# Performance work log

Hardware: AMD Instinct MI355X
Metric: run time of the kernel (lower is better)

The kernel has to match this reference:

```python
import jax, jax.numpy as jnp
import numpy as np

B = 8
M = 500_000
XSIZE = 128


def setup_inputs() -> dict:
    key = jax.random.key(0)
    k1, k2 = jax.random.split(key)
    indices = jax.random.randint(k1, (B, M, 3), 0, XSIZE, dtype=jnp.int32)
    values = jax.random.normal(k2, (B, M), dtype=jnp.float32)
    return {"indices": indices, "values": values, "xsize": XSIZE}


def reference(indices, values, xsize):
    # Batched scatter-add density accumulation (tensor_scatter_nd_add per sample)
    def scatter_one(idx, val):
        grid = jnp.zeros((xsize, xsize, xsize), dtype=val.dtype)
        return grid.at[idx[:, 0], idx[:, 1], idx[:, 2]].add(val)

    grid = jax.vmap(scatter_one)(indices, values)  # (B, X, X, X)

    # Adjacent voxel differences along each spatial axis
    d1 = grid[:, 1:, :, :] - grid[:, :-1, :, :]
    d2 = grid[:, :, 1:, :] - grid[:, :, :-1, :]
    d3 = grid[:, :, :, 1:] - grid[:, :, :, :-1]

    ax = (1, 2, 3)
    # Total variation loss: normalized by total voxel count xsize^3
    num_pixels = jnp.float32(xsize * xsize * xsize)
    tv = (jnp.sum(jnp.abs(d1), axis=ax)
          + jnp.sum(jnp.abs(d2), axis=ax)
          + jnp.sum(jnp.abs(d3), axis=ax)) / num_pixels

    # MSE smoothness loss: normalizer matches TF code (2*X*X - X - X)
    num_pairs = jnp.float32(2 * xsize * xsize - 2 * xsize)
    mse = (jnp.sum(jnp.square(d1), axis=ax)
           + jnp.sum(jnp.square(d2), axis=ax)
           + jnp.sum(jnp.square(d3), axis=ax)) / num_pairs

    return jnp.stack([tv, mse])  # (2, B)
```

## Files before the change

kernel.cpp:

```cpp
#include <hip/hip_runtime.h>
#include <stdint.h>

#define BATCH 8
#define MPTS 500000
#define NPTS (BATCH * MPTS)
#define NBQ 1024
#define TP 8192
#define NTILE ((NPTS + TP - 1) / TP)
#define NIFACE 304
#define NBND (BATCH * NIFACE)

template <int NT>
__device__ __forceinline__ void block_reduce2(float& tv, float& mse) {
    for (int off = 32; off > 0; off >>= 1) {
        tv  += __shfl_down(tv, off, 64);
        mse += __shfl_down(mse, off, 64);
    }
    __shared__ float stv[NT / 64], sms[NT / 64];
    int w = threadIdx.x >> 6, lane = threadIdx.x & 63;
    if (lane == 0) { stv[w] = tv; sms[w] = mse; }
    __syncthreads();
    if (threadIdx.x == 0) {
        float a = 0.f, m = 0.f;
        #pragma unroll
        for (int e = 0; e < NT / 64; ++e) { a += stv[e]; m += sms[e]; }
        tv = a; mse = m;
    }
}

__device__ __forceinline__ uint32_t pack_aux(int b, int i, int j, int k) {
    uint32_t q = ((uint32_t)b << 7) | ((uint32_t)(i >> 5) << 5) |
                 ((uint32_t)(j >> 5) << 3) | (uint32_t)(k >> 4);
    uint32_t l = ((uint32_t)(i & 31) << 9) | ((uint32_t)(j & 31) << 4) | (uint32_t)(k & 15);
    return (q << 14) | l;
}

__device__ __forceinline__ int gaddr(int s, int kl) {
    return s * 16 + (kl & 3) + ((((kl >> 2) ^ (s >> 1)) & 3) << 2);
}
__device__ __forceinline__ int goff(int s, int c) {
    return ((c ^ (s >> 1)) & 3) << 2;
}

__global__ void __launch_bounds__(1024) hist_k(const int* __restrict__ idx,
                                               uint32_t* __restrict__ hist,
                                               uint32_t* __restrict__ aux) {
    __shared__ uint32_t h[NBQ];
    h[threadIdx.x] = 0;
    __syncthreads();
    int tile = blockIdx.x;
    int p0 = tile * TP;
    int ng = min(TP, NPTS - p0) >> 2;
    for (int g = threadIdx.x; g < ng; g += 1024) {
        int p = p0 + g * 4;
        const int4* ip = (const int4*)(idx + (size_t)p * 3);
        int4 A = ip[0], B = ip[1], C = ip[2];
        int b = p / MPTS;
        uint32_t a0 = pack_aux(b, A.x, A.y, A.z);
        uint32_t a1 = pack_aux(b, A.w, B.x, B.y);
        uint32_t a2 = pack_aux(b, B.z, B.w, C.x);
        uint32_t a3 = pack_aux(b, C.y, C.z, C.w);
        *(uint4*)(aux + p) = make_uint4(a0, a1, a2, a3);
        atomicAdd(&h[a0 >> 14], 1u);
        atomicAdd(&h[a1 >> 14], 1u);
        atomicAdd(&h[a2 >> 14], 1u);
        atomicAdd(&h[a3 >> 14], 1u);
    }
    __syncthreads();
    hist[(size_t)tile * NBQ + threadIdx.x] = h[threadIdx.x];
}

__global__ void __launch_bounds__(64) scan_tiles_k(uint32_t* __restrict__ hist,
                                                   uint32_t* __restrict__ totals) {
    int q = blockIdx.x * 64 + threadIdx.x;
    uint32_t run = 0;
    for (int t0 = 0; t0 < NTILE; t0 += 16) {
        uint32_t vv[16];
        #pragma unroll
        for (int e = 0; e < 16; ++e) {
            int t = t0 + e;
            vv[e] = (t < NTILE) ? hist[(size_t)t * NBQ + q] : 0u;
        }
        #pragma unroll
        for (int e = 0; e < 16; ++e) {
            int t = t0 + e;
            if (t < NTILE) hist[(size_t)t * NBQ + q] = run;
            run += vv[e];
        }
    }
    totals[q] = run;
}

__global__ void __launch_bounds__(256) scan_base_k(const uint32_t* __restrict__ totals,
                                                   uint32_t* __restrict__ base) {
    __shared__ uint32_t ssum[256];
    uint32_t loc[4];
    int q0 = threadIdx.x * 4;
    uint32_t s = 0;
    #pragma unroll
    for (int e = 0; e < 4; ++e) { loc[e] = totals[q0 + e]; s += loc[e]; }
    ssum[threadIdx.x] = s;
    __syncthreads();
    for (int off = 1; off < 256; off <<= 1) {
        uint32_t v = 0;
        if (threadIdx.x >= off) v = ssum[threadIdx.x - off];
        __syncthreads();
        if (threadIdx.x >= off) ssum[threadIdx.x] += v;
        __syncthreads();
    }
    uint32_t run = threadIdx.x ? ssum[threadIdx.x - 1] : 0;
    #pragma unroll
    for (int e = 0; e < 4; ++e) { base[q0 + e] = run; run += loc[e]; }
}

__global__ void __launch_bounds__(1024, 8) reorder_k(const uint32_t* __restrict__ aux,
                                                     const float* __restrict__ val,
                                                     const uint32_t* __restrict__ hist,
                                                     const uint32_t* __restrict__ base,
                                                     uint32_t* __restrict__ rec) {
    __shared__ uint32_t h[NBQ];
    __shared__ uint32_t gb[NBQ];
    __shared__ uint32_t wtot[16];
    __shared__ uint16_t sq[TP];
    __shared__ uint32_t srt[TP];
    int tile = blockIdx.x;
    int p0 = tile * TP;
    int cnt = min(TP, NPTS - p0);
    h[threadIdx.x] = 0;
    __syncthreads();
    uint32_t a[8]; float v[8];
    #pragma unroll
    for (int e = 0; e < 8; ++e) {
        int r = threadIdx.x + e * 1024;
        if (r < cnt) {
            a[e] = aux[p0 + r];
            v[e] = val[p0 + r];
            atomicAdd(&h[a[e] >> 14], 1u);
        } else a[e] = 0xFFFFFFFFu;
    }
    __syncthreads();
    int q = threadIdx.x, lane = q & 63, wave = q >> 6;
    uint32_t cq = h[q];
    uint32_t inc = cq;
    #pragma unroll
    for (int off = 1; off < 64; off <<= 1) {
        uint32_t n = __shfl_up(inc, off, 64);
        if (lane >= off) inc += n;
    }
    if (lane == 63) wtot[wave] = inc;
    __syncthreads();
    if (q < 16) {
        uint32_t w = wtot[q];
        #pragma unroll
        for (int off = 1; off < 16; off <<= 1) {
            uint32_t n = __shfl_up(w, off, 16);
            if (q >= off) w += n;
        }
        wtot[q] = w;
    }
    __syncthreads();
    uint32_t lstart = (wave ? wtot[wave - 1] : 0u) + inc - cq;
    gb[q] = base[q] + hist[(size_t)tile * NBQ + q] - lstart;
    h[q] = lstart;
    __syncthreads();
    #pragma unroll
    for (int e = 0; e < 8; ++e) {
        if (a[e] != 0xFFFFFFFFu) {
            uint32_t qq = a[e] >> 14;
            uint32_t u = (__float_as_uint(v[e]) + 0x2000u) & 0xFFFFC000u;
            uint32_t pos = atomicAdd(&h[qq], 1u);
            srt[pos] = u | (a[e] & 16383u);
            sq[pos]  = (uint16_t)qq;
        }
    }
    __syncthreads();
    for (int t = threadIdx.x; t < cnt; t += 1024)
        rec[gb[sq[t]] + t] = srt[t];
}

__global__ void __launch_bounds__(1024, 8) accum_k(const uint32_t* __restrict__ rec,
                                                   const uint32_t* __restrict__ base,
                                                   const uint32_t* __restrict__ totals,
                                                   float* __restrict__ faces,
                                                   float2* __restrict__ pa) {
    __shared__ float g[16384];
    int qb = blockIdx.x;
    {
        float4 z = make_float4(0.f, 0.f, 0.f, 0.f);
        #pragma unroll
        for (int c = 0; c < 4; ++c)
            *(float4*)&g[(threadIdx.x + c * 1024) * 4] = z;
    }
    __syncthreads();
    uint32_t s0 = base[qb], cnt = totals[qb];
    for (uint32_t r = threadIdx.x; r < cnt; r += 1024) {
        uint32_t e = rec[s0 + r];
        int l = e & 16383;
        atomicAdd(&g[gaddr(l >> 4, l & 15)], __uint_as_float(e & 0xFFFFC000u));
    }
    __syncthreads();
    float tv = 0.f, mse = 0.f;
    {
        int s = threadIdx.x;
        int jl = s & 31, il = s >> 5;
        bool jin = jl < 31, iin = il < 31;
        float own[16];
        #pragma unroll
        for (int c = 0; c < 4; ++c)
            *(float4*)&own[c * 4] = *(const float4*)&g[s * 16 + goff(s, c)];
        #pragma unroll
        for (int k = 0; k < 15; ++k) {
            float d = own[k + 1] - own[k]; tv += fabsf(d); mse += d * d;
        }
        #pragma unroll
        for (int h = 0; h < 2; ++h) {
            if (jin) {
                float jn[8];
                *(float4*)&jn[0] = *(const float4*)&g[(s + 1) * 16 + goff(s + 1, 2 * h)];
                *(float4*)&jn[4] = *(const float4*)&g[(s + 1) * 16 + goff(s + 1, 2 * h + 1)];
                #pragma unroll
                for (int k = 0; k < 8; ++k) {
                    float d = jn[k] - own[8 * h + k]; tv += fabsf(d); mse += d * d;
                }
            }
            if (iin) {
                float inb[8];
                *(float4*)&inb[0] = *(const float4*)&g[(s + 32) * 16 + goff(s + 32, 2 * h)];
                *(float4*)&inb[4] = *(const float4*)&g[(s + 32) * 16 + goff(s + 32, 2 * h + 1)];
                #pragma unroll
                for (int k = 0; k < 8; ++k) {
                    float d = inb[k] - own[8 * h + k]; tv += fabsf(d); mse += d * d;
                }
            }
        }
    }
    {
        float* f = faces + (size_t)qb * 4096;
        int t = threadIdx.x;
        if (t < 512) {
            int hi = t >> 4, lo = t & 15;
            f[t]        = g[gaddr(hi, lo)];
            f[512 + t]  = g[gaddr(992 + hi, lo)];
            f[1024 + t] = g[gaddr(hi * 32, lo)];
            f[1536 + t] = g[gaddr(hi * 32 + 31, lo)];
        }
        f[2048 + t] = g[gaddr(t, 0)];
        f[3072 + t] = g[gaddr(t, 15)];
    }
    block_reduce2<1024>(tv, mse);
    if (threadIdx.x == 0) pa[qb] = make_float2(tv, mse);
}

__global__ void __launch_bounds__(256) boundary_k(const float* __restrict__ faces,
                                                  float2* __restrict__ pb) {
    int x = blockIdx.x;
    int b = x / NIFACE;
    int r = x - b * NIFACE;
    int qA, qB, fA, fB, elems;
    if (r < 96) {
        int s = r >> 5, u = (r >> 3) & 3, w = r & 7;
        qA = (b << 7) | (s << 5) | (u << 3) | w; qB = qA + 32;
        fA = 512; fB = 0; elems = 512;
    } else if (r < 192) {
        int r2 = r - 96;
        int s = r2 >> 5, u = (r2 >> 3) & 3, w = r2 & 7;
        qA = (b << 7) | (u << 5) | (s << 3) | w; qB = qA + 8;
        fA = 1536; fB = 1024; elems = 512;
    } else {
        int r2 = r - 192;
        int s = r2 >> 4, u = (r2 >> 2) & 3, v = r2 & 3;
        qA = (b << 7) | (u << 5) | (v << 3) | s; qB = qA + 1;
        fA = 3072; fB = 2048; elems = 1024;
    }
    const float* pA = faces + (size_t)qA * 4096 + fA;
    const float* pB = faces + (size_t)qB * 4096 + fB;
    float tv = 0.f, mse = 0.f;
    for (int e = threadIdx.x; e < elems; e += 256) {
        float d = pB[e] - pA[e];
        tv += fabsf(d); mse += d * d;
    }
    block_reduce2<256>(tv, mse);
    if (threadIdx.x == 0) pb[x] = make_float2(tv, mse);
}

__global__ void __launch_bounds__(256) final_k(const float2* __restrict__ pa,
                                               const float2* __restrict__ pb,
                                               float* __restrict__ out) {
    int b = blockIdx.x;
    float tv = 0.f, mse = 0.f;
    const float2* a = pa + (size_t)b * (NBQ / BATCH);
    for (int i = threadIdx.x; i < NBQ / BATCH; i += 256) { float2 v = a[i]; tv += v.x; mse += v.y; }
    const float2* p = pb + (size_t)b * NIFACE;
    for (int i = threadIdx.x; i < NIFACE; i += 256) { float2 v = p[i]; tv += v.x; mse += v.y; }
    block_reduce2<256>(tv, mse);
    if (threadIdx.x == 0) {
        out[b]     = tv  * (1.f / 2097152.f);
        out[8 + b] = mse * (1.f / 32512.f);
    }
}

extern "C" void kernel_launch(void* const* d_in, const int* in_sizes, int n_in,
                              void* d_out, int out_size, void* d_ws, size_t ws_size,
                              hipStream_t stream) {
    const int*   indices = (const int*)d_in[0];
    const float* values  = (const float*)d_in[1];
    float*       out     = (float*)d_out;

    uint32_t* hist   = (uint32_t*)d_ws;
    uint32_t* totals = hist + (size_t)NTILE * NBQ;
    uint32_t* base   = totals + NBQ;
    float2*   pa     = (float2*)(base + NBQ);
    float2*   pb     = pa + NBQ;
    uint32_t* rec    = (uint32_t*)(pb + NBND);
    float*    faces  = (float*)(rec + NPTS);
    uint32_t* aux    = (uint32_t*)faces;

    hist_k      <<<NTILE, 1024, 0, stream>>>(indices, hist, aux);
    scan_tiles_k<<<16,    64,   0, stream>>>(hist, totals);
    scan_base_k <<<1,     256,  0, stream>>>(totals, base);
    reorder_k   <<<NTILE, 1024, 0, stream>>>(aux, values, hist, base, rec);
    accum_k     <<<NBQ,   1024, 0, stream>>>(rec, base, totals, faces, pa);
    boundary_k  <<<NBND,  256,  0, stream>>>(faces, pb);
    final_k     <<<BATCH, 256,  0, stream>>>(pa, pb, out);
}
```

Baseline: 158.3 us.

## Fuse histogram and reorder into tile-local sort, drop global scans

Histogram, two scan kernels and reorder become one sort_k. It sorts each tile locally by bucket in shared memory, writes the tile contiguously with vector stores, and records per-tile bucket offsets. accum_k now gathers each bucket's segments across all tiles: up to 512 tiles, each split between two threads, read sequentially. This removes the aux round trip, the global scans and the scattered writes, and cuts the launch count. In exchange, reads in accum_k become many short per-thread serial loops with uneven lengths.

```diff
diff --git a/kernel.cpp b/kernel.cpp
--- a/kernel.cpp
+++ b/kernel.cpp
@@ -7,6 +7,7 @@
 #define NBQ 1024
 #define TP 8192
 #define NTILE ((NPTS + TP - 1) / TP)
+#define HROW (NBQ + 1)
 #define NIFACE 304
 #define NBND (BATCH * NIFACE)
 
@@ -42,86 +43,12 @@
     return ((c ^ (s >> 1)) & 3) << 2;
 }
 
-__global__ void __launch_bounds__(1024) hist_k(const int* __restrict__ idx,
-                                               uint32_t* __restrict__ hist,
-                                               uint32_t* __restrict__ aux) {
+__global__ void __launch_bounds__(1024, 8) sort_k(const int* __restrict__ idx,
+                                                  const float* __restrict__ val,
+                                                  uint32_t* __restrict__ hoff,
+                                                  uint32_t* __restrict__ rec) {
     __shared__ uint32_t h[NBQ];
-    h[threadIdx.x] = 0;
-    __syncthreads();
-    int tile = blockIdx.x;
-    int p0 = tile * TP;
-    int ng = min(TP, NPTS - p0) >> 2;
-    for (int g = threadIdx.x; g < ng; g += 1024) {
-        int p = p0 + g * 4;
-        const int4* ip = (const int4*)(idx + (size_t)p * 3);
-        int4 A = ip[0], B = ip[1], C = ip[2];
-        int b = p / MPTS;
-        uint32_t a0 = pack_aux(b, A.x, A.y, A.z);
-        uint32_t a1 = pack_aux(b, A.w, B.x, B.y);
-        uint32_t a2 = pack_aux(b, B.z, B.w, C.x);
-        uint32_t a3 = pack_aux(b, C.y, C.z, C.w);
-        *(uint4*)(aux + p) = make_uint4(a0, a1, a2, a3);
-        atomicAdd(&h[a0 >> 14], 1u);
-        atomicAdd(&h[a1 >> 14], 1u);
-        atomicAdd(&h[a2 >> 14], 1u);
-        atomicAdd(&h[a3 >> 14], 1u);
-    }
-    __syncthreads();
-    hist[(size_t)tile * NBQ + threadIdx.x] = h[threadIdx.x];
-}
-
-__global__ void __launch_bounds__(64) scan_tiles_k(uint32_t* __restrict__ hist,
-                                                   uint32_t* __restrict__ totals) {
-    int q = blockIdx.x * 64 + threadIdx.x;
-    uint32_t run = 0;
-    for (int t0 = 0; t0 < NTILE; t0 += 16) {
-        uint32_t vv[16];
-        #pragma unroll
-        for (int e = 0; e < 16; ++e) {
-            int t = t0 + e;
-            vv[e] = (t < NTILE) ? hist[(size_t)t * NBQ + q] : 0u;
-        }
-        #pragma unroll
-        for (int e = 0; e < 16; ++e) {
-            int t = t0 + e;
-            if (t < NTILE) hist[(size_t)t * NBQ + q] = run;
-            run += vv[e];
-        }
-    }
-    totals[q] = run;
-}
-
-__global__ void __launch_bounds__(256) scan_base_k(const uint32_t* __restrict__ totals,
-                                                   uint32_t* __restrict__ base) {
-    __shared__ uint32_t ssum[256];
-    uint32_t loc[4];
-    int q0 = threadIdx.x * 4;
-    uint32_t s = 0;
-    #pragma unroll
-    for (int e = 0; e < 4; ++e) { loc[e] = totals[q0 + e]; s += loc[e]; }
-    ssum[threadIdx.x] = s;
-    __syncthreads();
-    for (int off = 1; off < 256; off <<= 1) {
-        uint32_t v = 0;
-        if (threadIdx.x >= off) v = ssum[threadIdx.x - off];
-        __syncthreads();
-        if (threadIdx.x >= off) ssum[threadIdx.x] += v;
-        __syncthreads();
-    }
-    uint32_t run = threadIdx.x ? ssum[threadIdx.x - 1] : 0;
-    #pragma unroll
-    for (int e = 0; e < 4; ++e) { base[q0 + e] = run; run += loc[e]; }
-}
-
-__global__ void __launch_bounds__(1024, 8) reorder_k(const uint32_t* __restrict__ aux,
-                                                     const float* __restrict__ val,
-                                                     const uint32_t* __restrict__ hist,
-                                                     const uint32_t* __restrict__ base,
-                                                     uint32_t* __restrict__ rec) {
-    __shared__ uint32_t h[NBQ];
-    __shared__ uint32_t gb[NBQ];
     __shared__ uint32_t wtot[16];
-    __shared__ uint16_t sq[TP];
     __shared__ uint32_t srt[TP];
     int tile = blockIdx.x;
     int p0 = tile * TP;
@@ -129,14 +56,25 @@
     h[threadIdx.x] = 0;
     __syncthreads();
     uint32_t a[8]; float v[8];
+    int ng = cnt >> 2;
     #pragma unroll
-    for (int e = 0; e < 8; ++e) {
-        int r = threadIdx.x + e * 1024;
-        if (r < cnt) {
-            a[e] = aux[p0 + r];
-            v[e] = val[p0 + r];
-            atomicAdd(&h[a[e] >> 14], 1u);
-        } else a[e] = 0xFFFFFFFFu;
+    for (int e = 0; e < 2; ++e) {
+        int g = threadIdx.x + e * 1024;
+        if (g < ng) {
+            int p = p0 + g * 4;
+            const int4* ip = (const int4*)(idx + (size_t)p * 3);
+            int4 A = ip[0], B = ip[1], C = ip[2];
+            float4 V = *(const float4*)(val + p);
+            int b = p / MPTS;
+            a[4*e+0] = pack_aux(b, A.x, A.y, A.z); v[4*e+0] = V.x;
+            a[4*e+1] = pack_aux(b, A.w, B.x, B.y); v[4*e+1] = V.y;
+            a[4*e+2] = pack_aux(b, B.z, B.w, C.x); v[4*e+2] = V.z;
+            a[4*e+3] = pack_aux(b, C.y, C.z, C.w); v[4*e+3] = V.w;
+            #pragma unroll
+            for (int u = 0; u < 4; ++u) atomicAdd(&h[a[4*e+u] >> 14], 1u);
+        } else {
+            a[4*e+0] = a[4*e+1] = a[4*e+2] = a[4*e+3] = 0xFFFFFFFFu;
+        }
     }
     __syncthreads();
     int q = threadIdx.x, lane = q & 63, wave = q >> 6;
@@ -160,7 +98,8 @@
     }
     __syncthreads();
     uint32_t lstart = (wave ? wtot[wave - 1] : 0u) + inc - cq;
-    gb[q] = base[q] + hist[(size_t)tile * NBQ + q] - lstart;
+    hoff[(size_t)tile * HROW + q] = lstart;
+    if (q == 0) hoff[(size_t)tile * HROW + NBQ] = (uint32_t)cnt;
     h[q] = lstart;
     __syncthreads();
     #pragma unroll
@@ -168,19 +107,17 @@
         if (a[e] != 0xFFFFFFFFu) {
             uint32_t qq = a[e] >> 14;
             uint32_t u = (__float_as_uint(v[e]) + 0x2000u) & 0xFFFFC000u;
-            uint32_t pos = atomicAdd(&h[qq], 1u);
-            srt[pos] = u | (a[e] & 16383u);
-            sq[pos]  = (uint16_t)qq;
-        }
-    }
-    __syncthreads();
-    for (int t = threadIdx.x; t < cnt; t += 1024)
-        rec[gb[sq[t]] + t] = srt[t];
+            srt[atomicAdd(&h[qq], 1u)] = u | (a[e] & 16383u);
+        }
+    }
+    __syncthreads();
+    uint4* recq = (uint4*)(rec + (size_t)tile * TP);
+    const uint4* sr4 = (const uint4*)srt;
+    for (int s = threadIdx.x; s < (cnt >> 2); s += 1024) recq[s] = sr4[s];
 }
 
 __global__ void __launch_bounds__(1024, 8) accum_k(const uint32_t* __restrict__ rec,
-                                                   const uint32_t* __restrict__ base,
-                                                   const uint32_t* __restrict__ totals,
+                                                   const uint32_t* __restrict__ hoff,
                                                    float* __restrict__ faces,
                                                    float2* __restrict__ pa) {
     __shared__ float g[16384];
@@ -192,11 +129,21 @@
             *(float4*)&g[(threadIdx.x + c * 1024) * 4] = z;
     }
     __syncthreads();
-    uint32_t s0 = base[qb], cnt = totals[qb];
-    for (uint32_t r = threadIdx.x; r < cnt; r += 1024) {
-        uint32_t e = rec[s0 + r];
-        int l = e & 16383;
-        atomicAdd(&g[gaddr(l >> 4, l & 15)], __uint_as_float(e & 0xFFFFC000u));
+    {
+        int t = threadIdx.x & 511, half = threadIdx.x >> 9;
+        if (t < NTILE) {
+            const uint32_t* row = hoff + (size_t)t * HROW;
+            uint32_t s0 = row[qb], s1 = row[qb + 1];
+            uint32_t mid = s0 + ((s1 - s0) >> 1);
+            uint32_t lo = half ? mid : s0;
+            uint32_t hi = half ? s1 : mid;
+            const uint32_t* rp = rec + (size_t)t * TP;
+            for (uint32_t r = lo; r < hi; ++r) {
+                uint32_t e = rp[r];
+                int l = e & 16383;
+                atomicAdd(&g[gaddr(l >> 4, l & 15)], __uint_as_float(e & 0xFFFFC000u));
+            }
+        }
     }
     __syncthreads();
     float tv = 0.f, mse = 0.f;
@@ -213,23 +160,23 @@
             float d = own[k + 1] - own[k]; tv += fabsf(d); mse += d * d;
         }
         #pragma unroll
-        for (int h = 0; h < 2; ++h) {
+        for (int hh = 0; hh < 2; ++hh) {
             if (jin) {
                 float jn[8];
-                *(float4*)&jn[0] = *(const float4*)&g[(s + 1) * 16 + goff(s + 1, 2 * h)];
-                *(float4*)&jn[4] = *(const float4*)&g[(s + 1) * 16 + goff(s + 1, 2 * h + 1)];
+                *(float4*)&jn[0] = *(const float4*)&g[(s + 1) * 16 + goff(s + 1, 2 * hh)];
+                *(float4*)&jn[4] = *(const float4*)&g[(s + 1) * 16 + goff(s + 1, 2 * hh + 1)];
                 #pragma unroll
                 for (int k = 0; k < 8; ++k) {
-                    float d = jn[k] - own[8 * h + k]; tv += fabsf(d); mse += d * d;
+                    float d = jn[k] - own[8 * hh + k]; tv += fabsf(d); mse += d * d;
                 }
             }
             if (iin) {
                 float inb[8];
-                *(float4*)&inb[0] = *(const float4*)&g[(s + 32) * 16 + goff(s + 32, 2 * h)];
-                *(float4*)&inb[4] = *(const float4*)&g[(s + 32) * 16 + goff(s + 32, 2 * h + 1)];
+                *(float4*)&inb[0] = *(const float4*)&g[(s + 32) * 16 + goff(s + 32, 2 * hh)];
+                *(float4*)&inb[4] = *(const float4*)&g[(s + 32) * 16 + goff(s + 32, 2 * hh + 1)];
                 #pragma unroll
                 for (int k = 0; k < 8; ++k) {
-                    float d = inb[k] - own[8 * h + k]; tv += fabsf(d); mse += d * d;
+                    float d = inb[k] - own[8 * hh + k]; tv += fabsf(d); mse += d * d;
                 }
             }
         }
@@ -306,20 +253,14 @@
     const float* values  = (const float*)d_in[1];
     float*       out     = (float*)d_out;
 
-    uint32_t* hist   = (uint32_t*)d_ws;
-    uint32_t* totals = hist + (size_t)NTILE * NBQ;
-    uint32_t* base   = totals + NBQ;
-    float2*   pa     = (float2*)(base + NBQ);
-    float2*   pb     = pa + NBQ;
-    uint32_t* rec    = (uint32_t*)(pb + NBND);
-    float*    faces  = (float*)(rec + NPTS);
-    uint32_t* aux    = (uint32_t*)faces;
-
-    hist_k      <<<NTILE, 1024, 0, stream>>>(indices, hist, aux);
-    scan_tiles_k<<<16,    64,   0, stream>>>(hist, totals);
-    scan_base_k <<<1,     256,  0, stream>>>(totals, base);
-    reorder_k   <<<NTILE, 1024, 0, stream>>>(aux, values, hist, base, rec);
-    accum_k     <<<NBQ,   1024, 0, stream>>>(rec, base, totals, faces, pa);
-    boundary_k  <<<NBND,  256,  0, stream>>>(faces, pb);
-    final_k     <<<BATCH, 256,  0, stream>>>(pa, pb, out);
-}
+    uint32_t* hoff  = (uint32_t*)d_ws;
+    float2*   pa    = (float2*)(hoff + (size_t)NTILE * HROW);
+    float2*   pb    = pa + NBQ;
+    uint32_t* rec   = (uint32_t*)(pb + NBND);
+    float*    faces = (float*)(rec + NPTS);
+
+    sort_k    <<<NTILE, 1024, 0, stream>>>(indices, values, hoff, rec);
+    accum_k   <<<NBQ,   1024, 0, stream>>>(rec, hoff, faces, pa);
+    boundary_k<<<NBND,  256,  0, stream>>>(faces, pb);
+    final_k   <<<BATCH, 256,  0, stream>>>(pa, pb, out);
+}
```

Measured after the change: 147.7 us. 1.07x faster.
